# Kernel optimization log

Hardware: AMD Instinct MI355X
Metric: run time of the kernel (lower is better)

The kernel has to match this reference:

```python
import jax, jax.numpy as jnp
import numpy as np
from jax.scipy.special import erfinv

N_CHUNKS = 64
D = 128          # input_dim
O = 256          # output_dim
B = 4096         # batch (batch_last)
P = D // 2       # number of 2D pairs

def get_borders_cdf_grid(n):
    # CDF (Gaussian-quantile) spaced grid borders; clip probs to keep endpoints finite
    p = jnp.clip(jnp.arange(n + 1, dtype=jnp.float32) / n, 0.5 / n, 1.0 - 0.5 / n)
    return jnp.sqrt(2.0) * erfinv(2.0 * p - 1.0)

BORDERS = get_borders_cdf_grid(N_CHUNKS)  # (n_chunks+1,)


def setup_inputs() -> dict:
    key = jax.random.key(0)
    ks = jax.random.split(key, 5)
    s = 1.0 / np.sqrt(D)
    return {
        "x": jax.random.normal(ks[0], (D, B), dtype=jnp.float32),
        "weight_lmKAN": jnp.ones((1,), dtype=jnp.float32),
        "apply_relu_linear": 1,
        "func_parameter": jax.random.uniform(ks[1], (N_CHUNKS + 1, N_CHUNKS + 1, O, P), minval=-s, maxval=s, dtype=jnp.float32),
        "scale_parameters": jnp.ones((D,), dtype=jnp.float32),
        "bias_parameters": jnp.zeros((D,), dtype=jnp.float32),
        "W_linear": jax.random.uniform(ks[2], (O, D), minval=-s, maxval=s, dtype=jnp.float32),
        "bias_linear": jax.random.uniform(ks[3], (O,), minval=-s, maxval=s, dtype=jnp.float32),
    }


def lmkan_2d(fp, x):
    """2D bucketized grid lookup + bilinear interpolation.
    fp: (G, G, O, P) with G = n_chunks+1; x: (D, B) -> out (O, B)."""
    n = fp.shape[0] - 1
    pairs = x.reshape(P, 2, -1)                      # adjacent-channel pairs
    eps = 1e-6
    x1 = jnp.clip(pairs[:, 0], BORDERS[0], BORDERS[-1] - eps)  # (P, B)
    x2 = jnp.clip(pairs[:, 1], BORDERS[0], BORDERS[-1] - eps)
    i = jnp.clip(jnp.searchsorted(BORDERS, x1, side='right') - 1, 0, n - 1)
    j = jnp.clip(jnp.searchsorted(BORDERS, x2, side='right') - 1, 0, n - 1)
    t1 = (x1 - BORDERS[i]) / (BORDERS[i + 1] - BORDERS[i])      # (P, B) in [0,1)
    t2 = (x2 - BORDERS[j]) / (BORDERS[j + 1] - BORDERS[j])
    pidx = jnp.arange(P)[:, None]                    # (P, 1) -> broadcasts to (P, B)

    def corner(ii, jj, w):
        g = fp[ii, jj, :, pidx]                      # gather -> (P, B, O)
        return jnp.einsum('pb,pbo->ob', w, g)

    return (corner(i,     j,     (1.0 - t1) * (1.0 - t2))
          + corner(i + 1, j,     t1 * (1.0 - t2))
          + corner(i,     j + 1, (1.0 - t1) * t2)
          + corner(i + 1, j + 1, t1 * t2))


def reference(x, weight_lmKAN, apply_relu_linear, func_parameter, scale_parameters, bias_parameters, W_linear, bias_linear):
    # relu_last=True branch of the original forward
    linear_out = W_linear @ x + bias_linear[:, None]         # (O, B)
    if apply_relu_linear:
        linear_out = jax.nn.relu(linear_out)
    xs = x * scale_parameters[:, None] + bias_parameters[:, None]  # apply_scale / apply_bias
    # apply_tanh=False
    lmkan_out = lmkan_2d(func_parameter, xs)                 # (O, B)
    return 1.0 * linear_out + weight_lmKAN * lmkan_out
```

## Files before the change

### kernel.cpp

```cpp
#include <hip/hip_runtime.h>
#include <hip/hip_fp16.h>


#define NB 4096
#define ND 128
#define NO 256
#define NP 64
#define NG 65
#define PANEL 16384

__device__ __forceinline__ int bsearch65(const float* B, float v) {
  int lo = 0, hi = 65;
  while (lo < hi) {
    int m = (lo + hi) >> 1;
    if (B[m] <= v) lo = m + 1; else hi = m;
  }
  int i = lo - 1;
  return i < 0 ? 0 : (i > 63 ? 63 : i);
}

__global__ __launch_bounds__(128) void lmkan_transpose(
    const float* __restrict__ src, __half* __restrict__ dst) {
  const int panel = blockIdx.x;
  const int t = threadIdx.x;
  const float* s = src + (size_t)panel * PANEL;
  __half* d = dst + (size_t)panel * PANEL;
  const int o0 = 2 * t;
  const float4* ra = reinterpret_cast<const float4*>(s + (size_t)o0 * 64);
  const float4* rb = reinterpret_cast<const float4*>(s + (size_t)(o0 + 1) * 64);
#pragma unroll 4
  for (int pc = 0; pc < 16; ++pc) {
    float4 a = ra[pc];
    float4 b = rb[pc];
    *reinterpret_cast<__half2*>(d + (size_t)(4 * pc + 0) * NO + o0) = __floats2half2_rn(a.x, b.x);
    *reinterpret_cast<__half2*>(d + (size_t)(4 * pc + 1) * NO + o0) = __floats2half2_rn(a.y, b.y);
    *reinterpret_cast<__half2*>(d + (size_t)(4 * pc + 2) * NO + o0) = __floats2half2_rn(a.z, b.z);
    *reinterpret_cast<__half2*>(d + (size_t)(4 * pc + 3) * NO + o0) = __floats2half2_rn(a.w, b.w);
  }
}

__device__ __forceinline__ void fma4(float acc[4], float w, uint2 v) {
  __half2 h0 = *reinterpret_cast<__half2*>(&v.x);
  __half2 h1 = *reinterpret_cast<__half2*>(&v.y);
  float2 f0 = __half22float2(h0);
  float2 f1 = __half22float2(h1);
  acc[0] = fmaf(w, f0.x, acc[0]);
  acc[1] = fmaf(w, f0.y, acc[1]);
  acc[2] = fmaf(w, f1.x, acc[2]);
  acc[3] = fmaf(w, f1.y, acc[3]);
}

template <int MODE>
__global__ __launch_bounds__(64) void lmkan_gather(
    const float* __restrict__ x, const float* __restrict__ scale,
    const float* __restrict__ biasp, const float* __restrict__ W,
    const float* __restrict__ bias_l, const float* __restrict__ wlm_p,
    const int* __restrict__ relu_p, const void* __restrict__ table,
    float* __restrict__ out) {
  const int b = blockIdx.x;
  const int t = threadIdx.x;

  __shared__ float borders[66];
  __shared__ __align__(16) float xcol[ND];
  __shared__ int pbase[NP];
  __shared__ float4 pw[NP];

  for (int k = t; k < 65; k += 64) {
    float pk = fminf(fmaxf((float)k * (1.0f / 64.0f), 0.0078125f), 0.9921875f);
    borders[k] = 1.41421356237309515f * erfinvf(2.0f * pk - 1.0f);
  }
  xcol[t]      = x[(size_t)t * NB + b];
  xcol[t + 64] = x[(size_t)(t + 64) * NB + b];
  __syncthreads();

  {
    const int p = t;
    float x1 = xcol[2 * p]     * scale[2 * p]     + biasp[2 * p];
    float x2 = xcol[2 * p + 1] * scale[2 * p + 1] + biasp[2 * p + 1];
    const float lo = borders[0];
    const float hi = borders[64] - 1e-6f;
    x1 = fminf(fmaxf(x1, lo), hi);
    x2 = fminf(fmaxf(x2, lo), hi);
    int i = bsearch65(borders, x1);
    int j = bsearch65(borders, x2);
    float t1 = (x1 - borders[i]) / (borders[i + 1] - borders[i]);
    float t2 = (x2 - borders[j]) / (borders[j + 1] - borders[j]);
    pbase[p] = i * NG + j;
    pw[p] = make_float4((1.0f - t1) * (1.0f - t2),
                        t1 * (1.0f - t2),
                        (1.0f - t1) * t2,
                        t1 * t2);
  }
  __syncthreads();

  float acc[4] = {0.0f, 0.0f, 0.0f, 0.0f};

  if (MODE == 0) {
    const __half* fpt = reinterpret_cast<const __half*>(table);
#pragma unroll 4
    for (int p = 0; p < NP; ++p) {
      int base = pbase[p];
      float4 w = pw[p];
      const __half* q = fpt + ((size_t)base * NP + p) * NO + 4 * t;
      uint2 v00 = *reinterpret_cast<const uint2*>(q);
      uint2 v10 = *reinterpret_cast<const uint2*>(q + 65 * PANEL);
      uint2 v01 = *reinterpret_cast<const uint2*>(q + PANEL);
      uint2 v11 = *reinterpret_cast<const uint2*>(q + 66 * PANEL);
      fma4(acc, w.x, v00);
      fma4(acc, w.y, v10);
      fma4(acc, w.z, v01);
      fma4(acc, w.w, v11);
    }
  } else {
    const float* fp = reinterpret_cast<const float*>(table);
    for (int p = 0; p < NP; ++p) {
      int base = pbase[p];
      float4 w = pw[p];
#pragma unroll
      for (int k = 0; k < 4; ++k) {
        size_t r = ((size_t)base * NO + (4 * t + k)) * NP + p;
        float v = w.x * fp[r] + w.y * fp[r + 65 * PANEL] +
                  w.z * fp[r + PANEL] + w.w * fp[r + 66 * PANEL];
        acc[k] += v;
      }
    }
  }

  const float wlm = wlm_p[0];
  const int rl = relu_p[0];
  const float4* xc4 = reinterpret_cast<const float4*>(xcol);
#pragma unroll
  for (int k = 0; k < 4; ++k) {
    const int o = 4 * t + k;
    const float4* wr = reinterpret_cast<const float4*>(W + (size_t)o * ND);
    float s = 0.0f;
#pragma unroll 8
    for (int d4 = 0; d4 < ND / 4; ++d4) {
      float4 wv = wr[d4];
      float4 xv = xc4[d4];
      s = fmaf(wv.x, xv.x, s);
      s = fmaf(wv.y, xv.y, s);
      s = fmaf(wv.z, xv.z, s);
      s = fmaf(wv.w, xv.w, s);
    }
    s += bias_l[o];
    if (rl) s = fmaxf(s, 0.0f);
    out[(size_t)o * NB + b] = s + wlm * acc[k];
  }
}

extern "C" void kernel_launch(void* const* d_in, const int* in_sizes, int n_in,
                              void* d_out, int out_size, void* d_ws, size_t ws_size,
                              hipStream_t stream) {
  const float* x     = reinterpret_cast<const float*>(d_in[0]);
  const float* wlm   = reinterpret_cast<const float*>(d_in[1]);
  const int*   relu  = reinterpret_cast<const int*>(d_in[2]);
  const float* fp    = reinterpret_cast<const float*>(d_in[3]);
  const float* scale = reinterpret_cast<const float*>(d_in[4]);
  const float* biasp = reinterpret_cast<const float*>(d_in[5]);
  const float* W     = reinterpret_cast<const float*>(d_in[6]);
  const float* bl    = reinterpret_cast<const float*>(d_in[7]);
  float* out = reinterpret_cast<float*>(d_out);

  const size_t need = (size_t)NG * NG * PANEL * sizeof(__half);
  if (ws_size >= need) {
    __half* fpt = reinterpret_cast<__half*>(d_ws);
    lmkan_transpose<<<NG * NG, 128, 0, stream>>>(fp, fpt);
    lmkan_gather<0><<<NB, 64, 0, stream>>>(x, scale, biasp, W, bl, wlm, relu, fpt, out);
  } else {
    lmkan_gather<1><<<NB, 64, 0, stream>>>(x, scale, biasp, W, bl, wlm, relu, fp, out);
  }
}
```

Baseline: 225.2 us.

## Split gather over four waves per batch column with 16-byte loads and shared reduction

The fp16 gather kernel grows from one 64-thread wave to four waves per batch column. Each wave handles 16 pairs, and each half-wave covers one row of corners using 16-byte loads over 8 outputs. Partial sums are combined with a cross-half shuffle and a shared-memory reduction across the waves, and the linear dot product now runs one output per thread. This raises memory-level parallelism and shortens the serial per-thread loop over 64 pairs, at the cost of extra shared memory, a barrier, and a reduction.

```diff
diff --git a/kernel.cpp b/kernel.cpp
--- a/kernel.cpp
+++ b/kernel.cpp
@@ -39,41 +39,43 @@
   }
 }
 
-__device__ __forceinline__ void fma4(float acc[4], float w, uint2 v) {
-  __half2 h0 = *reinterpret_cast<__half2*>(&v.x);
-  __half2 h1 = *reinterpret_cast<__half2*>(&v.y);
-  float2 f0 = __half22float2(h0);
-  float2 f1 = __half22float2(h1);
-  acc[0] = fmaf(w, f0.x, acc[0]);
-  acc[1] = fmaf(w, f0.y, acc[1]);
-  acc[2] = fmaf(w, f1.x, acc[2]);
-  acc[3] = fmaf(w, f1.y, acc[3]);
-}
-
-template <int MODE>
-__global__ __launch_bounds__(64) void lmkan_gather(
+__device__ __forceinline__ void fma8(float acc[8], float w, uint4 v) {
+  const __half2* h = reinterpret_cast<const __half2*>(&v);
+#pragma unroll
+  for (int k = 0; k < 4; ++k) {
+    float2 f = __half22float2(h[k]);
+    acc[2 * k]     = fmaf(w, f.x, acc[2 * k]);
+    acc[2 * k + 1] = fmaf(w, f.y, acc[2 * k + 1]);
+  }
+}
+
+__global__ __launch_bounds__(256) void lmkan_gather4(
     const float* __restrict__ x, const float* __restrict__ scale,
     const float* __restrict__ biasp, const float* __restrict__ W,
     const float* __restrict__ bias_l, const float* __restrict__ wlm_p,
-    const int* __restrict__ relu_p, const void* __restrict__ table,
+    const int* __restrict__ relu_p, const __half* __restrict__ fpt,
     float* __restrict__ out) {
   const int b = blockIdx.x;
   const int t = threadIdx.x;
+  const int w = t >> 6;
+  const int l = t & 63;
+  const int h = l >> 5;
+  const int L = l & 31;
 
   __shared__ float borders[66];
   __shared__ __align__(16) float xcol[ND];
   __shared__ int pbase[NP];
   __shared__ float4 pw[NP];
-
-  for (int k = t; k < 65; k += 64) {
-    float pk = fminf(fmaxf((float)k * (1.0f / 64.0f), 0.0078125f), 0.9921875f);
-    borders[k] = 1.41421356237309515f * erfinvf(2.0f * pk - 1.0f);
-  }
-  xcol[t]      = x[(size_t)t * NB + b];
-  xcol[t + 64] = x[(size_t)(t + 64) * NB + b];
-  __syncthreads();
-
-  {
+  __shared__ float lm[4][NO];
+
+  if (t < 65) {
+    float pk = fminf(fmaxf((float)t * (1.0f / 64.0f), 0.0078125f), 0.9921875f);
+    borders[t] = 1.41421356237309515f * erfinvf(2.0f * pk - 1.0f);
+  }
+  if (t < ND) xcol[t] = x[(size_t)t * NB + b];
+  __syncthreads();
+
+  if (t < NP) {
     const int p = t;
     float x1 = xcol[2 * p]     * scale[2 * p]     + biasp[2 * p];
     float x2 = xcol[2 * p + 1] * scale[2 * p + 1] + biasp[2 * p + 1];
@@ -93,36 +95,97 @@
   }
   __syncthreads();
 
-  float acc[4] = {0.0f, 0.0f, 0.0f, 0.0f};
-
-  if (MODE == 0) {
-    const __half* fpt = reinterpret_cast<const __half*>(table);
-#pragma unroll 4
-    for (int p = 0; p < NP; ++p) {
-      int base = pbase[p];
-      float4 w = pw[p];
-      const __half* q = fpt + ((size_t)base * NP + p) * NO + 4 * t;
-      uint2 v00 = *reinterpret_cast<const uint2*>(q);
-      uint2 v10 = *reinterpret_cast<const uint2*>(q + 65 * PANEL);
-      uint2 v01 = *reinterpret_cast<const uint2*>(q + PANEL);
-      uint2 v11 = *reinterpret_cast<const uint2*>(q + 66 * PANEL);
-      fma4(acc, w.x, v00);
-      fma4(acc, w.y, v10);
-      fma4(acc, w.z, v01);
-      fma4(acc, w.w, v11);
-    }
-  } else {
-    const float* fp = reinterpret_cast<const float*>(table);
-    for (int p = 0; p < NP; ++p) {
-      int base = pbase[p];
-      float4 w = pw[p];
-#pragma unroll
-      for (int k = 0; k < 4; ++k) {
-        size_t r = ((size_t)base * NO + (4 * t + k)) * NP + p;
-        float v = w.x * fp[r] + w.y * fp[r + 65 * PANEL] +
-                  w.z * fp[r + PANEL] + w.w * fp[r + 66 * PANEL];
-        acc[k] += v;
-      }
+  float acc[8] = {0, 0, 0, 0, 0, 0, 0, 0};
+  const int p0 = w * 16;
+#pragma unroll 8
+  for (int pi = 0; pi < 16; ++pi) {
+    const int p = p0 + pi;
+    const int base = pbase[p] + h * NG;
+    const float4 wv = pw[p];
+    const float wA = h ? wv.y : wv.x;
+    const float wB = h ? wv.w : wv.z;
+    const __half* q = fpt + ((size_t)base * NP + p) * NO + 8 * L;
+    uint4 v0 = *reinterpret_cast<const uint4*>(q);
+    uint4 v1 = *reinterpret_cast<const uint4*>(q + PANEL);
+    fma8(acc, wA, v0);
+    fma8(acc, wB, v1);
+  }
+#pragma unroll
+  for (int k = 0; k < 8; ++k) acc[k] += __shfl_xor(acc[k], 32, 64);
+  if (l < 32) {
+#pragma unroll
+    for (int k = 0; k < 8; ++k) lm[w][8 * L + k] = acc[k];
+  }
+  __syncthreads();
+
+  const int o = t;
+  float lmsum = lm[0][o] + lm[1][o] + lm[2][o] + lm[3][o];
+  const float4* wr = reinterpret_cast<const float4*>(W + (size_t)o * ND);
+  const float4* xc4 = reinterpret_cast<const float4*>(xcol);
+  float s = 0.0f;
+#pragma unroll 8
+  for (int d4 = 0; d4 < ND / 4; ++d4) {
+    float4 wv = wr[d4];
+    float4 xv = xc4[d4];
+    s = fmaf(wv.x, xv.x, s);
+    s = fmaf(wv.y, xv.y, s);
+    s = fmaf(wv.z, xv.z, s);
+    s = fmaf(wv.w, xv.w, s);
+  }
+  s += bias_l[o];
+  if (relu_p[0]) s = fmaxf(s, 0.0f);
+  out[(size_t)o * NB + b] = s + wlm_p[0] * lmsum;
+}
+
+__global__ __launch_bounds__(64) void lmkan_gather_direct(
+    const float* __restrict__ x, const float* __restrict__ scale,
+    const float* __restrict__ biasp, const float* __restrict__ W,
+    const float* __restrict__ bias_l, const float* __restrict__ wlm_p,
+    const int* __restrict__ relu_p, const float* __restrict__ fp,
+    float* __restrict__ out) {
+  const int b = blockIdx.x;
+  const int t = threadIdx.x;
+
+  __shared__ float borders[66];
+  __shared__ __align__(16) float xcol[ND];
+  __shared__ int pbase[NP];
+  __shared__ float4 pw[NP];
+
+  for (int k = t; k < 65; k += 64) {
+    float pk = fminf(fmaxf((float)k * (1.0f / 64.0f), 0.0078125f), 0.9921875f);
+    borders[k] = 1.41421356237309515f * erfinvf(2.0f * pk - 1.0f);
+  }
+  xcol[t]      = x[(size_t)t * NB + b];
+  xcol[t + 64] = x[(size_t)(t + 64) * NB + b];
+  __syncthreads();
+
+  {
+    const int p = t;
+    float x1 = xcol[2 * p]     * scale[2 * p]     + biasp[2 * p];
+    float x2 = xcol[2 * p + 1] * scale[2 * p + 1] + biasp[2 * p + 1];
+    const float lo = borders[0];
+    const float hi = borders[64] - 1e-6f;
+    x1 = fminf(fmaxf(x1, lo), hi);
+    x2 = fminf(fmaxf(x2, lo), hi);
+    int i = bsearch65(borders, x1);
+    int j = bsearch65(borders, x2);
+    float t1 = (x1 - borders[i]) / (borders[i + 1] - borders[i]);
+    float t2 = (x2 - borders[j]) / (borders[j + 1] - borders[j]);
+    pbase[p] = i * NG + j;
+    pw[p] = make_float4((1.0f - t1) * (1.0f - t2), t1 * (1.0f - t2),
+                        (1.0f - t1) * t2, t1 * t2);
+  }
+  __syncthreads();
+
+  float acc[4] = {0, 0, 0, 0};
+  for (int p = 0; p < NP; ++p) {
+    int base = pbase[p];
+    float4 wv = pw[p];
+#pragma unroll
+    for (int k = 0; k < 4; ++k) {
+      size_t r = ((size_t)base * NO + (4 * t + k)) * NP + p;
+      acc[k] += wv.x * fp[r] + wv.y * fp[r + 65 * PANEL] +
+                wv.z * fp[r + PANEL] + wv.w * fp[r + 66 * PANEL];
     }
   }
 
@@ -166,8 +229,8 @@
   if (ws_size >= need) {
     __half* fpt = reinterpret_cast<__half*>(d_ws);
     lmkan_transpose<<<NG * NG, 128, 0, stream>>>(fp, fpt);
-    lmkan_gather<0><<<NB, 64, 0, stream>>>(x, scale, biasp, W, bl, wlm, relu, fpt, out);
+    lmkan_gather4<<<NB, 256, 0, stream>>>(x, scale, biasp, W, bl, wlm, relu, fpt, out);
   } else {
-    lmkan_gather<1><<<NB, 64, 0, stream>>>(x, scale, biasp, W, bl, wlm, relu, fp, out);
-  }
-}
+    lmkan_gather_direct<<<NB, 64, 0, stream>>>(x, scale, biasp, W, bl, wlm, relu, fp, out);
+  }
+}
```

New measurement: 227.1 us. Within noise of the previous version (+0.9%).
